# Kernel tuning notes

Measured on AMD Instinct MI355X. Metric: run time of the kernel, lower is better.

Reference implementation:

```python
import jax, jax.numpy as jnp
import numpy as np
import math

EPS = 1e-8
LN_EPS = 1e-5
B, S, E, NH = 2, 2048, 1024, 4
DH = E // NH


def setup_inputs() -> dict:
    key = jax.random.key(0)
    ks = jax.random.split(key, 7)
    std_g = math.sqrt(2.0 / (5.0 * 3 * E))
    return {
        "q": jax.random.normal(ks[0], (B, S, E), dtype=jnp.float32),
        "k": jax.random.normal(ks[1], (B, S, E), dtype=jnp.float32),
        "v": jax.random.normal(ks[2], (B, S, E), dtype=jnp.float32),
        "igate_w": jax.random.normal(ks[3], (NH, 3 * E), dtype=jnp.float32) * std_g,
        "igate_b": jax.random.normal(ks[4], (NH,), dtype=jnp.float32) * 0.1,
        "fgate_w": jax.random.normal(ks[5], (NH, 3 * E), dtype=jnp.float32) * std_g,
        "fgate_b": jnp.linspace(3.4, 6.0, NH, dtype=jnp.float32),
        "out_w": jnp.zeros((E,), dtype=jnp.float32),  # residual affine weight (scale = 1 + out_w)
    }


def _mlstm_cell(q, k, v, igate_w, igate_b, fgate_w, fgate_b, out_w):
    Bq, Sq, Eq = q.shape
    # gate pre-activations from concatenated q,k,v: [B,S,NH]
    if_in = jnp.concatenate([q, k, v], axis=-1)
    ig = jnp.einsum("bsf,hf->bsh", if_in, igate_w) + igate_b
    fg = jnp.einsum("bsf,hf->bsh", if_in, fgate_w) + fgate_b
    ig = jnp.transpose(ig, (0, 2, 1))[..., None]  # [B,NH,S,1]
    fg = jnp.transpose(fg, (0, 2, 1))[..., None]  # [B,NH,S,1]

    # split heads: [B,NH,S,DH]
    qh = q.reshape(Bq, Sq, NH, DH).transpose(0, 2, 1, 3)
    kh = k.reshape(Bq, Sq, NH, DH).transpose(0, 2, 1, 3)
    vh = v.reshape(Bq, Sq, NH, DH).transpose(0, 2, 1, 3)

    # cumulative log forget gates -> causal decay matrix (log space)
    log_fg = jax.nn.log_sigmoid(fg)                           # [B,NH,S,1]
    cs = jnp.cumsum(log_fg, axis=2)                           # [B,NH,S,1]
    cs_shift = jnp.concatenate([jnp.zeros_like(cs[:, :, :1]), cs[:, :, :-1]], axis=2)
    # log_fg_matrix[i,j] = cumsum[i] - cumsum[j-1], masked causal
    logfg_mat = cs - jnp.swapaxes(cs_shift, -2, -1)           # [B,NH,S,S]
    ltr = jnp.tril(jnp.ones((Sq, Sq), dtype=bool))
    logfg_mat = jnp.where(ltr, logfg_mat, -jnp.inf)
    log_D = logfg_mat + jnp.swapaxes(ig, -2, -1)              # + igate row broadcast [B,NH,1,S]

    max_log_D = jnp.max(log_D, axis=-1, keepdims=True)        # [B,NH,S,1]
    D = jnp.exp(log_D - max_log_D)                            # stabilized decay matrix

    qk = jnp.einsum("bhsd,bhtd->bhst", qh, kh / math.sqrt(DH))
    C = qk * D
    sum_C_abs = jnp.abs(jnp.sum(C, axis=-1, keepdims=True))
    normaliser = jnp.maximum(sum_C_abs, jnp.exp(-max_log_D))  # robust normalizer
    C_norm = C / (normaliser + EPS)
    h = jnp.einsum("bhst,bhtd->bhsd", C_norm, vh)             # [B,NH,S,DH]

    # MultiHeadLayerNorm == group_norm with NH groups, per-channel residual weight
    mean = jnp.mean(h, axis=-1, keepdims=True)
    var = jnp.mean((h - mean) ** 2, axis=-1, keepdims=True)
    h_norm = (h - mean) / jnp.sqrt(var + LN_EPS)
    scale = (1.0 + out_w).reshape(1, NH, 1, DH)
    h_norm = h_norm * scale

    return h_norm.transpose(0, 2, 1, 3).reshape(Bq, Sq, Eq)


def reference(q, k, v, igate_w, igate_b, fgate_w, fgate_b, out_w):
    return _mlstm_cell(q, k, v, igate_w, igate_b, fgate_w, fgate_b, out_w)
```

## Files before the change

### kernel.cpp

```cpp
#include <hip/hip_runtime.h>
#include <hip/hip_bf16.h>
#include <math.h>

#define Bb  2
#define Ss  2048
#define Ee  1024
#define NHh 4
#define DHh 256
#define BH  (Bb*NHh)
#define TI  64
#define TJ  32
#define NT2 (Ss/TI)
#define NJT (Ss/TJ)

typedef short        s8v   __attribute__((ext_vector_type(8)));
typedef float        f4v   __attribute__((ext_vector_type(4)));
typedef float        f16v  __attribute__((ext_vector_type(16)));
typedef unsigned int u4v   __attribute__((ext_vector_type(4)));
typedef unsigned int u2v   __attribute__((ext_vector_type(2)));

__device__ inline unsigned pkbf2(float a, float b) {
    __hip_bfloat162 h2 = __float22bfloat162_rn(float2{a, b});
    unsigned u;
    __builtin_memcpy(&u, &h2, 4);
    return u;
}

__device__ inline void async16(const void* g, void* l) {
    __builtin_amdgcn_global_load_lds(
        (const __attribute__((address_space(1))) void*)g,
        (__attribute__((address_space(3))) void*)l, 16, 0, 0);
}

__global__ __launch_bounds__(256) void gates_prep_kernel(
    const float* __restrict__ q, const float* __restrict__ k, const float* __restrict__ v,
    const float* __restrict__ igw, const float* __restrict__ igb,
    const float* __restrict__ fgw, const float* __restrict__ fgb,
    float* __restrict__ ig_out, float* __restrict__ fg_out,
    unsigned short* __restrict__ Kimg, unsigned short* __restrict__ Vimg)
{
    int bidx = blockIdx.x;
    int tid = threadIdx.x;

    if (bidx >= 512) {
        int pidx = bidx - 512;
        int bh = pidx >> 6, jt = pidx & 63;
        int b = bh >> 2, h = bh & 3;
        int J0 = jt * TJ;
        const size_t hoff = (size_t)h * DHh;
        unsigned short* Kt = Kimg + (size_t)pidx * 1024 * 8;
        unsigned short* Vt = Vimg + (size_t)pidx * 1024 * 8;

        {
            int kR = tid >> 3, kc0 = tid & 7;
            const float* src = k + ((size_t)(b * Ss + J0 + kR)) * Ee + hoff;
#pragma unroll
            for (int p = 0; p < 4; p++) {
                int cc = kc0 + 8 * p;
                float4 x0 = ((const float4*)(src + cc * 8))[0];
                float4 x1 = ((const float4*)(src + cc * 8))[1];
                u4v wv;
                wv.x = pkbf2(x0.x, x0.y); wv.y = pkbf2(x0.z, x0.w);
                wv.z = pkbf2(x1.x, x1.y); wv.w = pkbf2(x1.z, x1.w);
                *(u4v*)&Kt[(kR * 32 + (cc ^ (kR & 7))) * 8] = wv;
            }
        }
        {
            int vdp = tid & 127, vjb = tid >> 7;
            int d0 = vdp * 2;
#pragma unroll
            for (int p = 0; p < 2; p++) {
                int jc = vjb + 2 * p;
                const float* vbase = v + ((size_t)(b * Ss + J0 + jc * 8)) * Ee + hoff + d0;
                float2 e0 = *(const float2*)(vbase);
                float2 e1 = *(const float2*)(vbase + Ee);
                float2 e2 = *(const float2*)(vbase + 2 * Ee);
                float2 e3 = *(const float2*)(vbase + 3 * Ee);
                float2 e4 = *(const float2*)(vbase + 4 * Ee);
                float2 e5 = *(const float2*)(vbase + 5 * Ee);
                float2 e6 = *(const float2*)(vbase + 6 * Ee);
                float2 e7 = *(const float2*)(vbase + 7 * Ee);
                int swz = jc ^ (vdp & 3);
                u4v w0, w1;
                w0.x = pkbf2(e0.x, e1.x); w0.y = pkbf2(e2.x, e3.x);
                w0.z = pkbf2(e4.x, e5.x); w0.w = pkbf2(e6.x, e7.x);
                w1.x = pkbf2(e0.y, e1.y); w1.y = pkbf2(e2.y, e3.y);
                w1.z = pkbf2(e4.y, e5.y); w1.w = pkbf2(e6.y, e7.y);
                *(u4v*)&Vt[(d0 * 4 + swz) * 8] = w0;
                *(u4v*)&Vt[((d0 + 1) * 4 + swz) * 8] = w1;
            }
        }
        return;
    }

    int sc = bidx >> 1, hp = bidx & 1;
    __shared__ float wl[4][3072];
    __shared__ float pw[4][4];

#pragma unroll
    for (int c = 0; c < 4; c++) {
        int h = hp * 2 + (c >> 1);
        const float* src = ((c & 1) ? fgw : igw) + (size_t)h * 3 * Ee;
        for (int idx = tid * 4; idx < 3 * Ee; idx += 1024)
            *(float4*)&wl[c][idx] = *(const float4*)(src + idx);
    }
    __syncthreads();

    int c4 = tid * 4;
    int w = tid >> 6, lane = tid & 63;

    for (int ss = 0; ss < 16; ss++) {
        int bs = sc * 16 + ss;
        float4 q4v = *(const float4*)(q + (size_t)bs * Ee + c4);
        float4 k4v = *(const float4*)(k + (size_t)bs * Ee + c4);
        float4 v4v = *(const float4*)(v + (size_t)bs * Ee + c4);
        float red[4];
#pragma unroll
        for (int c = 0; c < 4; c++) {
            const float* wc = wl[c];
            float4 wq = *(const float4*)&wc[c4];
            float4 wk = *(const float4*)&wc[Ee + c4];
            float4 wv = *(const float4*)&wc[2 * Ee + c4];
            float x = q4v.x*wq.x + q4v.y*wq.y + q4v.z*wq.z + q4v.w*wq.w
                    + k4v.x*wk.x + k4v.y*wk.y + k4v.z*wk.z + k4v.w*wk.w
                    + v4v.x*wv.x + v4v.y*wv.y + v4v.z*wv.z + v4v.w*wv.w;
            for (int off = 32; off > 0; off >>= 1) x += __shfl_down(x, off, 64);
            red[c] = x;
        }
        __syncthreads();
        if (lane == 0) {
#pragma unroll
            for (int c = 0; c < 4; c++) pw[w][c] = red[c];
        }
        __syncthreads();
        if (tid < 4) {
            float t = pw[0][tid] + pw[1][tid] + pw[2][tid] + pw[3][tid];
            int h = hp * 2 + (tid >> 1);
            int b = bs >> 11, s = bs & 2047;
            size_t o = ((size_t)(b * NHh + h)) * Ss + s;
            if (tid & 1) fg_out[o] = t + fgb[h];
            else         ig_out[o] = t + igb[h];
        }
    }
}

#define CHUNK 8
__global__ __launch_bounds__(256) void scan_kernel(
    const float* __restrict__ ig, const float* __restrict__ fg,
    float* __restrict__ a_out, float* __restrict__ M_out, float* __restrict__ nf_out)
{
    int bh = blockIdx.x;
    int tid = threadIdx.x;
    const float* igp = ig + (size_t)bh * Ss;
    const float* fgp = fg + (size_t)bh * Ss;
    int s0 = tid * CHUNK;

    float ls[CHUNK], cs[CHUNK];
    float tot = 0.f;
#pragma unroll
    for (int c = 0; c < CHUNK; c++) {
        float x = fgp[s0 + c];
        float l = fminf(x, 0.f) - log1pf(expf(-fabsf(x)));
        ls[c] = l; tot += l; cs[c] = tot;
    }
    __shared__ float sc[256];
    sc[tid] = tot; __syncthreads();
    for (int off = 1; off < 256; off <<= 1) {
        float add = (tid >= off) ? sc[tid - off] : 0.f;
        __syncthreads();
        sc[tid] += add;
        __syncthreads();
    }
    float excl = sc[tid] - tot;

    float av[CHUNK], pmax[CHUNK];
    float tmax = -INFINITY;
#pragma unroll
    for (int c = 0; c < CHUNK; c++) {
        float csf  = excl + cs[c];
        float csm1 = csf - ls[c];
        float a = igp[s0 + c] - csm1;
        av[c] = a;
        tmax = fmaxf(tmax, a);
        pmax[c] = tmax;
        cs[c] = csf;
    }
    __shared__ float sm[256];
    sm[tid] = tmax; __syncthreads();
    for (int off = 1; off < 256; off <<= 1) {
        float other = (tid >= off) ? sm[tid - off] : -INFINITY;
        __syncthreads();
        sm[tid] = fmaxf(sm[tid], other);
        __syncthreads();
    }
    float emax = (tid > 0) ? sm[tid - 1] : -INFINITY;
#pragma unroll
    for (int c = 0; c < CHUNK; c++) {
        float M = fmaxf(emax, pmax[c]);
        size_t o = (size_t)bh * Ss + s0 + c;
        a_out[o]  = av[c];
        M_out[o]  = M;
        nf_out[o] = expf(-cs[c] - M);
    }
}

__global__ __launch_bounds__(256, 2) void mlstm_dbuf(
    const float* __restrict__ qp,
    const unsigned short* __restrict__ Kimg, const unsigned short* __restrict__ Vimg,
    const float* __restrict__ a_ws, const float* __restrict__ M_ws,
    float* __restrict__ outF, float* __restrict__ Hpart, float* __restrict__ rsbuf)
{
    int bidx = blockIdx.x;
    int qd = bidx >> 8, u = bidx & 255;
    int bh = u & 7;
    int r  = u >> 3;
    int T  = (qd < 2) ? (31 - r) : r;
    int sg = qd;
    int b = bh >> 2, h = bh & 3;
    int I0 = T * TI;
    int tid = threadIdx.x;

    const int tot = 2 * T + 2;
    const int jt_beg = (sg * tot) / 4;
    const int jt_end = ((sg + 1) * tot) / 4;
    const size_t hoff = (size_t)h * DHh;
    float* Hdst = (sg == 0) ? outF : (Hpart + (size_t)(sg - 1) * Bb * Ss * Ee);

    if (jt_beg >= jt_end) {
        float4 z = {0.f, 0.f, 0.f, 0.f};
        for (int t = tid; t < TI * 64; t += 256) {
            int r2 = t >> 6, c = t & 63;
            *(float4*)(Hdst + ((size_t)(b * Ss + I0 + r2)) * Ee + hoff + 4 * c) = z;
        }
        if (tid < TI) rsbuf[(size_t)sg * BH * Ss + (size_t)bh * Ss + I0 + tid] = 0.f;
        return;
    }

    __shared__ unsigned short KF[2][1024 * 8];
    __shared__ unsigned short VF[2][1024 * 8];
    __shared__ unsigned short PF[256 * 8];
    __shared__ float a_s[2][TJ];
    __shared__ float rs_s[TI];

    const int iq   = tid >> 6;
    const int lane = tid & 63;
    const int lm = lane & 15, q4 = lane >> 4;

    s8v qf[8];
    {
        const float* qrow = qp + ((size_t)(b * Ss + I0 + iq * 16 + lm)) * Ee + hoff;
#pragma unroll
        for (int ks = 0; ks < 8; ks++) {
            const float4* p = (const float4*)(qrow + ks * 32 + q4 * 8);
            float4 x0 = p[0], x1 = p[1];
            union { s8v v; unsigned u[4]; } rr;
            rr.u[0] = pkbf2(x0.x, x0.y);
            rr.u[1] = pkbf2(x0.z, x0.w);
            rr.u[2] = pkbf2(x1.x, x1.y);
            rr.u[3] = pkbf2(x1.z, x1.w);
            qf[ks] = rr.v;
        }
    }
    const int  i_row = I0 + iq * 16 + lm;
    const float Mi = M_ws[(size_t)bh * Ss + i_row];

    f4v acc[16];
#pragma unroll
    for (int t = 0; t < 16; t++) { acc[t][0]=0.f; acc[t][1]=0.f; acc[t][2]=0.f; acc[t][3]=0.f; }
    float rs_acc = 0.f;
    const float inv_sqrt_dh = 0.0625f;

    const unsigned short* Kb = Kimg + (size_t)(bh * NJT) * 1024 * 8;
    const unsigned short* Vb = Vimg + (size_t)(bh * NJT) * 1024 * 8;

    {
        const unsigned short* Kt = Kb + (size_t)jt_beg * 1024 * 8;
        const unsigned short* Vt = Vb + (size_t)jt_beg * 1024 * 8;
#pragma unroll
        for (int p = 0; p < 4; p++) {
            int cbase = (iq * 4 + p) * 64;
            async16(Kt + (size_t)(cbase + lane) * 8, &KF[0][cbase * 8]);
            async16(Vt + (size_t)(cbase + lane) * 8, &VF[0][cbase * 8]);
        }
        if (tid < TJ) a_s[0][tid] = a_ws[(size_t)bh * Ss + jt_beg * TJ + tid];
    }

    int cur = 0;
    for (int jt = jt_beg; jt < jt_end; jt++, cur ^= 1) {
        __syncthreads();

        if (jt + 1 < jt_end) {
            const unsigned short* Kt = Kb + (size_t)(jt + 1) * 1024 * 8;
            const unsigned short* Vt = Vb + (size_t)(jt + 1) * 1024 * 8;
#pragma unroll
            for (int p = 0; p < 4; p++) {
                int cbase = (iq * 4 + p) * 64;
                async16(Kt + (size_t)(cbase + lane) * 8, &KF[cur ^ 1][cbase * 8]);
                async16(Vt + (size_t)(cbase + lane) * 8, &VF[cur ^ 1][cbase * 8]);
            }
            if (tid < TJ) a_s[cur ^ 1][tid] = a_ws[(size_t)bh * Ss + (jt + 1) * TJ + tid];
        }
        const int J0 = jt * TJ;

        f4v c0 = {0.f, 0.f, 0.f, 0.f}, c1 = c0;
#pragma unroll
        for (int ks = 0; ks < 8; ks++) {
            int swzk = ((ks * 4 + q4) ^ (lm & 7)) * 8;
            s8v af0 = *(const s8v*)&KF[cur][(lm * 32) * 8 + swzk];
            s8v af1 = *(const s8v*)&KF[cur][((16 + lm) * 32) * 8 + swzk];
            c0 = __builtin_amdgcn_mfma_f32_16x16x32_bf16(af0, qf[ks], c0, 0, 0, 0);
            c1 = __builtin_amdgcn_mfma_f32_16x16x32_bf16(af1, qf[ks], c1, 0, 0, 0);
        }
        {
            float rsum = 0.f;
#pragma unroll
            for (int t = 0; t < 2; t++) {
                const f4v cc = t ? c1 : c0;
                const int jb = t * 16 + q4 * 4;
                float p[4];
#pragma unroll
                for (int rr = 0; rr < 4; rr++) {
                    int jg = J0 + jb + rr;
                    float pv = 0.f;
                    if (jg <= i_row) pv = cc[rr] * inv_sqrt_dh * __expf(a_s[cur][jb + rr] - Mi);
                    p[rr] = pv; rsum += pv;
                }
                u2v pwv;
                pwv.x = pkbf2(p[0], p[1]);
                pwv.y = pkbf2(p[2], p[3]);
                int kb = t * 2 + (q4 >> 1);
                *(u2v*)&PF[(iq * 64 + lm * 4 + (kb ^ (lm & 3))) * 8 + (q4 & 1) * 4] = pwv;
            }
            rsum += __shfl_xor(rsum, 16);
            rsum += __shfl_xor(rsum, 32);
            rs_acc += rsum;
        }
        s8v pa = *(const s8v*)&PF[(iq * 64 + lm * 4 + (q4 ^ (lm & 3))) * 8];

#pragma unroll
        for (int db = 0; db < 16; db++) {
            int d = db * 16 + lm;
            s8v vb = *(const s8v*)&VF[cur][(d * 4 + (q4 ^ ((d >> 1) & 3))) * 8];
            acc[db] = __builtin_amdgcn_mfma_f32_16x16x32_bf16(pa, vb, acc[db], 0, 0, 0);
        }
    }

    if (q4 == 0) rs_s[iq * 16 + lm] = rs_acc;
    __syncthreads();
    if (tid < TI)
        rsbuf[(size_t)sg * BH * Ss + (size_t)bh * Ss + I0 + tid] = rs_s[tid];

#pragma unroll
    for (int rr = 0; rr < 4; rr++) {
        float* row = Hdst + ((size_t)(b * Ss + I0 + iq * 16 + q4 * 4 + rr)) * Ee + hoff + lm;
#pragma unroll
        for (int db = 0; db < 16; db++)
            row[db * 16] = acc[db][rr];
    }
}

template<int PARTS>
__global__ __launch_bounds__(256, 4) void mlstm_fallback(
    const float* __restrict__ qp, const float* __restrict__ kp, const float* __restrict__ vp,
    const float* __restrict__ a_ws, const float* __restrict__ M_ws,
    float* __restrict__ outF, float* __restrict__ Hpart, float* __restrict__ rsbuf)
{
    int bidx = blockIdx.x;
    int bh, T, sg;
    if (PARTS == 1) {
        bh = bidx & 7; T = (NT2 - 1) - (bidx >> 3); sg = 0;
    } else {
        int qd = bidx >> 8, u = bidx & 255;
        bh = u & 7;
        int r = u >> 3;
        T  = qd ? r : (31 - r);
        sg = r & 1;
    }
    int b = bh >> 2, h = bh & 3;
    int I0 = T * TI;
    int tid = threadIdx.x;

    const int tot = 2 * T + 2;
    const int jt_beg = (sg * tot) / PARTS;
    const int jt_end = ((sg + 1) * tot) / PARTS;
    const size_t hoff = (size_t)h * DHh;
    float* Hdst = (sg == 0) ? outF : (Hpart + (size_t)(sg - 1) * Bb * Ss * Ee);

    if (jt_beg >= jt_end) {
        float4 z = {0.f, 0.f, 0.f, 0.f};
        for (int t = tid; t < TI * 64; t += 256) {
            int r2 = t >> 6, c = t & 63;
            *(float4*)(Hdst + ((size_t)(b * Ss + I0 + r2)) * Ee + hoff + 4 * c) = z;
        }
        if (tid < TI) rsbuf[(size_t)sg * BH * Ss + (size_t)bh * Ss + I0 + tid] = 0.f;
        return;
    }

    __shared__ unsigned short KF[1024 * 8];
    __shared__ unsigned short VF[1024 * 8];
    __shared__ unsigned short PF[256 * 8];
    __shared__ float a_s[TJ];
    __shared__ float rs_s[TI];

    const int iq   = tid >> 6;
    const int lane = tid & 63;
    const int lm = lane & 15, q4 = lane >> 4;
    const int m5 = lane & 31, hl = lane >> 5;

    s8v qf[8];
    {
        const float* qrow = qp + ((size_t)(b * Ss + I0 + iq * 16 + lm)) * Ee + hoff;
#pragma unroll
        for (int ks = 0; ks < 8; ks++) {
            const float4* p = (const float4*)(qrow + ks * 32 + q4 * 8);
            float4 x0 = p[0], x1 = p[1];
            union { s8v v; unsigned u[4]; } rr;
            rr.u[0] = pkbf2(x0.x, x0.y);
            rr.u[1] = pkbf2(x0.z, x0.w);
            rr.u[2] = pkbf2(x1.x, x1.y);
            rr.u[3] = pkbf2(x1.z, x1.w);
            qf[ks] = rr.v;
        }
    }
    const int  i_row = I0 + iq * 16 + lm;
    const float Mi = M_ws[(size_t)bh * Ss + i_row];

    f16v acc[4];
#pragma unroll
    for (int t = 0; t < 4; t++)
#pragma unroll
        for (int i = 0; i < 16; i++) acc[t][i] = 0.f;
    float rs_acc = 0.f;

    const float inv_sqrt_dh = 0.0625f;
    const int kR  = tid >> 3, kc0 = tid & 7;
    const int vdp = tid & 127, vjb = tid >> 7;

    for (int jt = jt_beg; jt < jt_end; jt++) {
        const int J0 = jt * TJ;
        __syncthreads();
        {
            const float* src = kp + ((size_t)(b * Ss + J0 + kR)) * Ee + hoff;
#pragma unroll
            for (int p = 0; p < 4; p++) {
                int cc = kc0 + 8 * p;
                float4 x0 = ((const float4*)(src + cc * 8))[0];
                float4 x1 = ((const float4*)(src + cc * 8))[1];
                u4v wv;
                wv.x = pkbf2(x0.x, x0.y); wv.y = pkbf2(x0.z, x0.w);
                wv.z = pkbf2(x1.x, x1.y); wv.w = pkbf2(x1.z, x1.w);
                *(u4v*)&KF[(kR * 32 + (cc ^ (kR & 7))) * 8] = wv;
            }
            int d0 = vdp * 2;
#pragma unroll
            for (int p = 0; p < 2; p++) {
                int jc = vjb + 2 * p;
                const float* vbase = vp + ((size_t)(b * Ss + J0 + jc * 8)) * Ee + hoff + d0;
                float2 e0 = *(const float2*)(vbase);
                float2 e1 = *(const float2*)(vbase + Ee);
                float2 e2 = *(const float2*)(vbase + 2 * Ee);
                float2 e3 = *(const float2*)(vbase + 3 * Ee);
                float2 e4 = *(const float2*)(vbase + 4 * Ee);
                float2 e5 = *(const float2*)(vbase + 5 * Ee);
                float2 e6 = *(const float2*)(vbase + 6 * Ee);
                float2 e7 = *(const float2*)(vbase + 7 * Ee);
                int swz = jc ^ (vdp & 3);
                u4v w0, w1;
                w0.x = pkbf2(e0.x, e1.x); w0.y = pkbf2(e2.x, e3.x);
                w0.z = pkbf2(e4.x, e5.x); w0.w = pkbf2(e6.x, e7.x);
                w1.x = pkbf2(e0.y, e1.y); w1.y = pkbf2(e2.y, e3.y);
                w1.z = pkbf2(e4.y, e5.y); w1.w = pkbf2(e6.y, e7.y);
                *(u4v*)&VF[(d0 * 4 + swz) * 8] = w0;
                *(u4v*)&VF[((d0 + 1) * 4 + swz) * 8] = w1;
            }
        }
        if (tid < TJ) a_s[tid] = a_ws[(size_t)bh * Ss + J0 + tid];
        __syncthreads();

        f4v c0 = {0.f, 0.f, 0.f, 0.f}, c1 = c0;
#pragma unroll
        for (int ks = 0; ks < 8; ks++) {
            int swzk = ((ks * 4 + q4) ^ (lm & 7)) * 8;
            s8v af0 = *(const s8v*)&KF[(lm * 32) * 8 + swzk];
            s8v af1 = *(const s8v*)&KF[((16 + lm) * 32) * 8 + swzk];
            c0 = __builtin_amdgcn_mfma_f32_16x16x32_bf16(af0, qf[ks], c0, 0, 0, 0);
            c1 = __builtin_amdgcn_mfma_f32_16x16x32_bf16(af1, qf[ks], c1, 0, 0, 0);
        }
        {
            float rsum = 0.f;
#pragma unroll
            for (int t = 0; t < 2; t++) {
                const f4v cc = t ? c1 : c0;
                const int jb = t * 16 + q4 * 4;
                float p[4];
#pragma unroll
                for (int rr = 0; rr < 4; rr++) {
                    int jg = J0 + jb + rr;
                    float pv = 0.f;
                    if (jg <= i_row) pv = cc[rr] * inv_sqrt_dh * __expf(a_s[jb + rr] - Mi);
                    p[rr] = pv; rsum += pv;
                }
                u2v pwv;
                pwv.x = pkbf2(p[0], p[1]);
                pwv.y = pkbf2(p[2], p[3]);
                int i = iq * 16 + lm;
                int kb = t * 2 + (q4 >> 1);
                *(u2v*)&PF[(i * 4 + (kb ^ ((i >> 1) & 3))) * 8 + (q4 & 1) * 4] = pwv;
            }
            rsum += __shfl_xor(rsum, 16);
            rsum += __shfl_xor(rsum, 32);
            rs_acc += rsum;
        }
        __syncthreads();

#pragma unroll
        for (int ks2 = 0; ks2 < 2; ks2++) {
            int swz2 = ((ks2 * 2 + hl) ^ ((m5 >> 1) & 3)) * 8;
            s8v pa0 = *(const s8v*)&PF[(m5 * 4) * 8 + swz2];
            s8v pa1 = *(const s8v*)&PF[((32 + m5) * 4) * 8 + swz2];
            s8v vb0 = *(const s8v*)&VF[((iq * 32 + m5) * 4) * 8 + swz2];
            s8v vb1 = *(const s8v*)&VF[(((iq + 4) * 32 + m5) * 4) * 8 + swz2];
            acc[0] = __builtin_amdgcn_mfma_f32_32x32x16_bf16(pa0, vb0, acc[0], 0, 0, 0);
            acc[1] = __builtin_amdgcn_mfma_f32_32x32x16_bf16(pa0, vb1, acc[1], 0, 0, 0);
            acc[2] = __builtin_amdgcn_mfma_f32_32x32x16_bf16(pa1, vb0, acc[2], 0, 0, 0);
            acc[3] = __builtin_amdgcn_mfma_f32_32x32x16_bf16(pa1, vb1, acc[3], 0, 0, 0);
        }
    }

    if (q4 == 0) rs_s[iq * 16 + lm] = rs_acc;
    __syncthreads();
    if (tid < TI)
        rsbuf[(size_t)sg * BH * Ss + (size_t)bh * Ss + I0 + tid] = rs_s[tid];

#pragma unroll
    for (int im = 0; im < 2; im++)
#pragma unroll
        for (int ns = 0; ns < 2; ns++) {
            const f16v av = acc[im * 2 + ns];
            const int col = (iq + 4 * ns) * 32 + m5;
#pragma unroll
            for (int rr = 0; rr < 16; rr++) {
                int row = I0 + im * 32 + (rr & 3) + 8 * (rr >> 2) + 4 * hl;
                Hdst[((size_t)(b * Ss + row)) * Ee + hoff + col] = av[rr];
            }
        }
}

template<int PARTS>
__global__ __launch_bounds__(256) void combine_kernel(
    const float* __restrict__ Hb, const float* __restrict__ rsbuf,
    const float* __restrict__ nf_ws, const float* __restrict__ out_w,
    float* __restrict__ outF)
{
    int rid = blockIdx.x * 4 + (threadIdx.x >> 6);
    int lane = threadIdx.x & 63;
    int bh = rid >> 11, s = rid & 2047;
    int b = bh >> 2, h = bh & 3;
    size_t base = ((size_t)(b * Ss + s)) * Ee + (size_t)h * DHh + lane * 4;
    float4 ha = *(const float4*)(outF + base);
    float rs = rsbuf[(size_t)bh * Ss + s];
#pragma unroll
    for (int k = 1; k < PARTS; k++) {
        float4 hb = *(const float4*)(Hb + (size_t)(k - 1) * Bb * Ss * Ee + base);
        ha.x += hb.x; ha.y += hb.y; ha.z += hb.z; ha.w += hb.w;
        rs += rsbuf[(size_t)k * BH * Ss + (size_t)bh * Ss + s];
    }
    float nfv = nf_ws[(size_t)bh * Ss + s];
    float invn = 1.f / (fmaxf(fabsf(rs), nfv) + 1e-8f);
    float4 x;
    x.x = ha.x * invn; x.y = ha.y * invn; x.z = ha.z * invn; x.w = ha.w * invn;
    float sx = x.x + x.y + x.z + x.w;
    float sq = x.x*x.x + x.y*x.y + x.z*x.z + x.w*x.w;
#pragma unroll
    for (int off = 1; off < 64; off <<= 1) {
        sx += __shfl_xor(sx, off);
        sq += __shfl_xor(sq, off);
    }
    float mean = sx * (1.f / DHh);
    float var  = sq * (1.f / DHh) - mean * mean;
    float rstd = rsqrtf(var + 1e-5f);
    float4 w4 = *(const float4*)(out_w + (size_t)h * DHh + lane * 4);
    float4 o;
    o.x = (x.x - mean) * rstd * (1.f + w4.x);
    o.y = (x.y - mean) * rstd * (1.f + w4.y);
    o.z = (x.z - mean) * rstd * (1.f + w4.z);
    o.w = (x.w - mean) * rstd * (1.f + w4.w);
    *(float4*)(outF + base) = o;
}

extern "C" void kernel_launch(void* const* d_in, const int* in_sizes, int n_in,
                              void* d_out, int out_size, void* d_ws, size_t ws_size,
                              hipStream_t stream) {
    const float* q   = (const float*)d_in[0];
    const float* k   = (const float*)d_in[1];
    const float* v   = (const float*)d_in[2];
    const float* igw = (const float*)d_in[3];
    const float* igb = (const float*)d_in[4];
    const float* fgw = (const float*)d_in[5];
    const float* fgb = (const float*)d_in[6];
    const float* ow  = (const float*)d_in[7];
    float* out = (float*)d_out;

    float* ws = (float*)d_ws;
    float* ig = ws;
    float* fg = ws + 16384;
    float* aa = ws + 32768;
    float* MM = ws + 49152;
    float* nf = ws + 65536;
    float* rsb = ws + 81920;
    const size_t base_f = 81920 + 65536;
    unsigned short* KimgP = (unsigned short*)(ws + base_f);
    const size_t img_u = (size_t)BH * NJT * 1024 * 8;
    unsigned short* VimgP = KimgP + img_u;
    float* HpartImg = (float*)(VimgP + img_u);
    float* HpartRaw = ws + base_f;
    const size_t HP = (size_t)Bb * Ss * Ee;

    const size_t need4  = base_f * 4 + 2 * img_u * 2 + 3 * HP * 4;
    const size_t need2  = base_f * 4 + 1 * HP * 4;

    if (ws_size >= need4) {
        gates_prep_kernel<<<1024, 256, 0, stream>>>(q, k, v, igw, igb, fgw, fgb,
                                                    ig, fg, KimgP, VimgP);
        scan_kernel<<<BH, 256, 0, stream>>>(ig, fg, aa, MM, nf);
        mlstm_dbuf<<<1024, 256, 0, stream>>>(q, KimgP, VimgP, aa, MM,
                                             out, HpartImg, rsb);
        combine_kernel<4><<<BH * Ss / 4, 256, 0, stream>>>(HpartImg, rsb, nf, ow, out);
    } else if (ws_size >= need2) {
        gates_prep_kernel<<<512, 256, 0, stream>>>(q, k, v, igw, igb, fgw, fgb,
                                                   ig, fg, nullptr, nullptr);
        scan_kernel<<<BH, 256, 0, stream>>>(ig, fg, aa, MM, nf);
        mlstm_fallback<2><<<512, 256, 0, stream>>>(q, k, v, aa, MM, out, HpartRaw, rsb);
        combine_kernel<2><<<BH * Ss / 4, 256, 0, stream>>>(HpartRaw, rsb, nf, ow, out);
    } else {
        gates_prep_kernel<<<512, 256, 0, stream>>>(q, k, v, igw, igb, fgw, fgb,
                                                   ig, fg, nullptr, nullptr);
        scan_kernel<<<BH, 256, 0, stream>>>(ig, fg, aa, MM, nf);
        mlstm_fallback<1><<<256, 256, 0, stream>>>(q, k, v, aa, MM, out, HpartRaw, rsb);
        combine_kernel<1><<<BH * Ss / 4, 256, 0, stream>>>(HpartRaw, rsb, nf, ow, out);
    }
}
```

Before: 200.7 us.

## Replace double-buffered K/V tiles with phased single-buffer loads and raise occupancy

The attention kernel drops its double-buffered K/V shared-memory tiles. It now loads the V tile while the QK MFMAs run, and loads the next K tile plus the gate values while the PV MFMAs run, with barriers between the two phases. This roughly halves LDS use, so launch bounds can ask for 4 blocks per CU instead of 2, letting all 1024 blocks be resident at once. It also wraps the MFMA loops in s_setprio to favour matrix issue. The cost is two barriers per tile and less prefetch distance, so latency hiding now relies on more resident blocks rather than on in-block buffering.

Result: slower. 223.8 us (+11.5%).

```diff
diff --git a/kernel.cpp b/kernel.cpp
--- a/kernel.cpp
+++ b/kernel.cpp
@@ -204,7 +204,7 @@
     }
 }
 
-__global__ __launch_bounds__(256, 2) void mlstm_dbuf(
+__global__ __launch_bounds__(256, 4) void mlstm_phase(
     const float* __restrict__ qp,
     const unsigned short* __restrict__ Kimg, const unsigned short* __restrict__ Vimg,
     const float* __restrict__ a_ws, const float* __restrict__ M_ws,
@@ -236,10 +236,10 @@
         return;
     }
 
-    __shared__ unsigned short KF[2][1024 * 8];
-    __shared__ unsigned short VF[2][1024 * 8];
+    __shared__ unsigned short KF[1024 * 8];
+    __shared__ unsigned short VF[1024 * 8];
     __shared__ unsigned short PF[256 * 8];
-    __shared__ float a_s[2][TJ];
+    __shared__ float a_s[TJ];
     __shared__ float rs_s[TI];
 
     const int iq   = tid >> 6;
@@ -272,45 +272,42 @@
 
     const unsigned short* Kb = Kimg + (size_t)(bh * NJT) * 1024 * 8;
     const unsigned short* Vb = Vimg + (size_t)(bh * NJT) * 1024 * 8;
+    const float* a_base = a_ws + (size_t)bh * Ss;
 
     {
         const unsigned short* Kt = Kb + (size_t)jt_beg * 1024 * 8;
-        const unsigned short* Vt = Vb + (size_t)jt_beg * 1024 * 8;
 #pragma unroll
         for (int p = 0; p < 4; p++) {
             int cbase = (iq * 4 + p) * 64;
-            async16(Kt + (size_t)(cbase + lane) * 8, &KF[0][cbase * 8]);
-            async16(Vt + (size_t)(cbase + lane) * 8, &VF[0][cbase * 8]);
-        }
-        if (tid < TJ) a_s[0][tid] = a_ws[(size_t)bh * Ss + jt_beg * TJ + tid];
-    }
-
-    int cur = 0;
-    for (int jt = jt_beg; jt < jt_end; jt++, cur ^= 1) {
-        __syncthreads();
-
-        if (jt + 1 < jt_end) {
-            const unsigned short* Kt = Kb + (size_t)(jt + 1) * 1024 * 8;
-            const unsigned short* Vt = Vb + (size_t)(jt + 1) * 1024 * 8;
+            async16(Kt + (size_t)(cbase + lane) * 8, &KF[cbase * 8]);
+        }
+        if (lane < 2)
+            async16(a_base + (size_t)jt_beg * TJ + iq * 8 + lane * 4, &a_s[iq * 8]);
+    }
+    __syncthreads();
+
+    for (int jt = jt_beg; jt < jt_end; jt++) {
+        {
+            const unsigned short* Vt = Vb + (size_t)jt * 1024 * 8;
 #pragma unroll
             for (int p = 0; p < 4; p++) {
                 int cbase = (iq * 4 + p) * 64;
-                async16(Kt + (size_t)(cbase + lane) * 8, &KF[cur ^ 1][cbase * 8]);
-                async16(Vt + (size_t)(cbase + lane) * 8, &VF[cur ^ 1][cbase * 8]);
-            }
-            if (tid < TJ) a_s[cur ^ 1][tid] = a_ws[(size_t)bh * Ss + (jt + 1) * TJ + tid];
+                async16(Vt + (size_t)(cbase + lane) * 8, &VF[cbase * 8]);
+            }
         }
         const int J0 = jt * TJ;
 
         f4v c0 = {0.f, 0.f, 0.f, 0.f}, c1 = c0;
+        __builtin_amdgcn_s_setprio(1);
 #pragma unroll
         for (int ks = 0; ks < 8; ks++) {
             int swzk = ((ks * 4 + q4) ^ (lm & 7)) * 8;
-            s8v af0 = *(const s8v*)&KF[cur][(lm * 32) * 8 + swzk];
-            s8v af1 = *(const s8v*)&KF[cur][((16 + lm) * 32) * 8 + swzk];
+            s8v af0 = *(const s8v*)&KF[(lm * 32) * 8 + swzk];
+            s8v af1 = *(const s8v*)&KF[((16 + lm) * 32) * 8 + swzk];
             c0 = __builtin_amdgcn_mfma_f32_16x16x32_bf16(af0, qf[ks], c0, 0, 0, 0);
             c1 = __builtin_amdgcn_mfma_f32_16x16x32_bf16(af1, qf[ks], c1, 0, 0, 0);
         }
+        __builtin_amdgcn_s_setprio(0);
         {
             float rsum = 0.f;
 #pragma unroll
@@ -322,7 +319,7 @@
                 for (int rr = 0; rr < 4; rr++) {
                     int jg = J0 + jb + rr;
                     float pv = 0.f;
-                    if (jg <= i_row) pv = cc[rr] * inv_sqrt_dh * __expf(a_s[cur][jb + rr] - Mi);
+                    if (jg <= i_row) pv = cc[rr] * inv_sqrt_dh * __expf(a_s[jb + rr] - Mi);
                     p[rr] = pv; rsum += pv;
                 }
                 u2v pwv;
@@ -337,12 +334,29 @@
         }
         s8v pa = *(const s8v*)&PF[(iq * 64 + lm * 4 + (q4 ^ (lm & 3))) * 8];
 
+        __syncthreads();
+
+        if (jt + 1 < jt_end) {
+            const unsigned short* Kt = Kb + (size_t)(jt + 1) * 1024 * 8;
+#pragma unroll
+            for (int p = 0; p < 4; p++) {
+                int cbase = (iq * 4 + p) * 64;
+                async16(Kt + (size_t)(cbase + lane) * 8, &KF[cbase * 8]);
+            }
+            if (lane < 2)
+                async16(a_base + (size_t)(jt + 1) * TJ + iq * 8 + lane * 4, &a_s[iq * 8]);
+        }
+
+        __builtin_amdgcn_s_setprio(1);
 #pragma unroll
         for (int db = 0; db < 16; db++) {
             int d = db * 16 + lm;
-            s8v vb = *(const s8v*)&VF[cur][(d * 4 + (q4 ^ ((d >> 1) & 3))) * 8];
+            s8v vb = *(const s8v*)&VF[(d * 4 + (q4 ^ ((d >> 1) & 3))) * 8];
             acc[db] = __builtin_amdgcn_mfma_f32_16x16x32_bf16(pa, vb, acc[db], 0, 0, 0);
         }
+        __builtin_amdgcn_s_setprio(0);
+
+        __syncthreads();
     }
 
     if (q4 == 0) rs_s[iq * 16 + lm] = rs_acc;
@@ -623,8 +637,8 @@
         gates_prep_kernel<<<1024, 256, 0, stream>>>(q, k, v, igw, igb, fgw, fgb,
                                                     ig, fg, KimgP, VimgP);
         scan_kernel<<<BH, 256, 0, stream>>>(ig, fg, aa, MM, nf);
-        mlstm_dbuf<<<1024, 256, 0, stream>>>(q, KimgP, VimgP, aa, MM,
-                                             out, HpartImg, rsb);
+        mlstm_phase<<<1024, 256, 0, stream>>>(q, KimgP, VimgP, aa, MM,
+                                              out, HpartImg, rsb);
         combine_kernel<4><<<BH * Ss / 4, 256, 0, stream>>>(HpartImg, rsb, nf, ow, out);
     } else if (ws_size >= need2) {
         gates_prep_kernel<<<512, 256, 0, stream>>>(q, k, v, igw, igb, fgw, fgb,
```
